# Kernel tuning notes

Hardware: AMD Instinct MI355X
Metric: run time of the kernel (lower is better)

The kernel has to match this reference:

```python
import jax, jax.numpy as jnp
import numpy as np

B, F, T = 4, 2048, 2048
CF, CT = 1024, 1024
H, DH = 16, 64
ALPHA = 1.0 / np.sqrt(DH).astype(np.float32)


def setup_inputs() -> dict:
    key = jax.random.key(0)
    ks = jax.random.split(key, 8)
    s = 0.02  # trunc_normal-ish init scale
    return {
        "from_tensor": jax.random.normal(ks[0], (B, F, CF), jnp.float32),
        "to_tensor": jax.random.normal(ks[1], (B, T, CT), jnp.float32),
        "mask": jax.random.randint(ks[2], (B, F, T), 0, 2, jnp.int32),
        "Wq": jax.random.normal(ks[3], (CF, H * DH), jnp.float32) * s,
        "bq": jnp.zeros((H * DH,), jnp.float32),
        "Wk": jax.random.normal(ks[4], (CT, H * DH), jnp.float32) * s,
        "bk": jnp.zeros((H * DH,), jnp.float32),
        "Wv": jax.random.normal(ks[5], (CT, H * DH), jnp.float32) * s,
        "bv": jnp.zeros((H * DH,), jnp.float32),
    }


def reference(from_tensor, to_tensor, mask, Wq, bq, Wk, bk, Wv, bv):
    # projections (nn.Linear with no activation)
    q = from_tensor @ Wq + bq          # [B,F,H*DH]
    k = to_tensor @ Wk + bk            # [B,T,H*DH]
    v = to_tensor @ Wv + bv            # [B,T,H*DH]
    q = q.reshape(B, F, H, DH)         # query: [..., F, H, DH]
    k = k.reshape(B, T, DH, H)         # key:   [..., T, DH, H]  (self._shape[::-1])
    v = v.reshape(B, T, H, DH)
    # score = transpose(q,-3,-2) @ transpose(k,-3,-1) * alpha -> [B,H,F,T]
    score = jnp.einsum("bfhd,btdh->bhft", q, k) * ALPHA
    if mask is not None:
        adder = (1.0 - mask[:, None].astype(score.dtype)) * -100000.0  # [B,1,F,T]
        score = score + adder
    probs = jax.nn.softmax(score, axis=-1)  # dropout p=0.0 -> identity
    # context = probs @ transpose(v,-3,-2), then transpose back: [B,F,H,DH]
    context = jnp.einsum("bhft,bthd->bfhd", probs, v)
    return context.reshape(B, F, H * DH)
```

## Files before the change

### kernel.cpp

```cpp
#include <hip/hip_runtime.h>
#include <type_traits>

typedef __bf16 bf16_t;
typedef __attribute__((ext_vector_type(8))) __bf16 bf16x8;
typedef __attribute__((ext_vector_type(4))) float f32x4;
typedef __attribute__((ext_vector_type(16))) float f32x16;

__device__ __forceinline__ void async16(const void* g, void* lds) {
  __builtin_amdgcn_global_load_lds((const __attribute__((address_space(1))) unsigned int*)g,
                                   (__attribute__((address_space(3))) unsigned int*)lds, 16, 0, 0);
}

__device__ __forceinline__ unsigned pk2(float lo, float hi) {
  unsigned short a = __builtin_bit_cast(unsigned short, (__bf16)lo);
  unsigned short b = __builtin_bit_cast(unsigned short, (__bf16)hi);
  return (unsigned)a | ((unsigned)b << 16);
}

__device__ __forceinline__ void plswap(unsigned& a, unsigned& b) {
#if __has_builtin(__builtin_amdgcn_permlane32_swap)
  auto r = __builtin_amdgcn_permlane32_swap((int)a, (int)b, false, false);
  a = (unsigned)r[0];
  b = (unsigned)r[1];
#else
  const bool hb = (threadIdx.x & 32) != 0;
  unsigned bx = (unsigned)__shfl_xor((int)b, 32);
  unsigned ax = (unsigned)__shfl_xor((int)a, 32);
  unsigned na = hb ? bx : a;
  unsigned nb = hb ? b : ax;
  a = na; b = nb;
#endif
}

__global__ __launch_bounds__(256) void pack_mask_kernel(const int* __restrict__ mask,
                                                        unsigned long long* __restrict__ mb) {
  const int lane = threadIdx.x & 63, w = threadIdx.x >> 6;
  for (int i = 0; i < 32; ++i) {
    size_t word = (size_t)blockIdx.x * 128 + (size_t)i * 4 + w;
    unsigned long long bits = __ballot(mask[word * 64 + lane] != 0);
    if (lane == 0) mb[word] = bits;
  }
}

__global__ __launch_bounds__(256) void cvt_bf16_kernel(const float* __restrict__ in, bf16_t* __restrict__ out) {
  size_t i = (size_t)blockIdx.x * 256 + threadIdx.x;
  const float4* in4 = (const float4*)in;
  float4 a = in4[i * 2], b = in4[i * 2 + 1];
  bf16x8 o;
  o[0] = (__bf16)a.x; o[1] = (__bf16)a.y; o[2] = (__bf16)a.z; o[3] = (__bf16)a.w;
  o[4] = (__bf16)b.x; o[5] = (__bf16)b.y; o[6] = (__bf16)b.z; o[7] = (__bf16)b.w;
  *(bf16x8*)(out + i * 8) = o;
}

__global__ __launch_bounds__(256) void wt_cvt_kernel(const float* __restrict__ Wq, const float* __restrict__ Wk,
                                                     const float* __restrict__ Wv, bf16_t* __restrict__ Wt) {
  const int z = blockIdx.z;
  const float* src = (z == 0) ? Wq : ((z == 1) ? Wk : Wv);
  const float sc = (z == 0) ? 0.18033688011112042f : 1.0f;
  bf16_t* dst = Wt + (size_t)z * 1024 * 1024;
  const int n = blockIdx.x * 64 + (threadIdx.x & 63);
  const int k8 = blockIdx.y * 4 + (threadIdx.x >> 6);
  bf16x8 o;
#pragma unroll
  for (int j = 0; j < 8; ++j) o[j] = (__bf16)(src[(size_t)(k8 * 8 + j) * 1024 + n] * sc);
  *(bf16x8*)(dst + (size_t)n * 1024 + k8 * 8) = o;
}

__global__ __launch_bounds__(256) void proj_kernel(const bf16_t* __restrict__ A, const bf16_t* __restrict__ Wt,
                                                   const float* __restrict__ bias, bf16_t* __restrict__ dst,
                                                   const int z, const float bscale) {
  __shared__ __align__(16) unsigned char smem[33792];
  bf16_t* se = (bf16_t*)smem;
  const int tid = threadIdx.x, lane = tid & 63, w = tid >> 6;
  const int m0 = blockIdx.x * 128, n0 = blockIdx.y * 128;
  const int wm = (w >> 1) * 64, wn = (w & 1) * 64;
  const int r = lane & 15, kq = lane >> 4;
  const int srow = lane >> 2, sslot = lane & 3;
  f32x4 acc[4][4] = {};

  auto stage = [&](int buf, int k0) {
    bf16_t* Ad = se + buf * 4096;
    bf16_t* Bd = se + 8192 + buf * 4096;
#pragma unroll
    for (int it = 0; it < 2; ++it) {
      const int c = it * 4 + w;
      const int row = c * 16 + srow;
      async16(A + (size_t)(m0 + row) * 1024 + k0 + ((sslot ^ (row & 3)) * 8), Ad + c * 512);
      async16(Wt + (size_t)(n0 + row) * 1024 + k0 + ((sslot ^ (row & 3)) * 8), Bd + c * 512);
    }
  };

  stage(0, 0);
  __syncthreads();
  for (int tile = 0; tile < 32; ++tile) {
    const int cur = tile & 1;
    if (tile < 31) stage(cur ^ 1, (tile + 1) * 32);
    const bf16_t* Al = se + cur * 4096;
    const bf16_t* Bl = se + 8192 + cur * 4096;
    bf16x8 af[4], bfr[4];
#pragma unroll
    for (int i = 0; i < 4; ++i) {
      const int ra = wm + i * 16 + r;
      af[i] = *(const bf16x8*)(Al + ra * 32 + ((kq ^ (ra & 3)) * 8));
      const int rb = wn + i * 16 + r;
      bfr[i] = *(const bf16x8*)(Bl + rb * 32 + ((kq ^ (rb & 3)) * 8));
    }
    __builtin_amdgcn_s_setprio(1);
#pragma unroll
    for (int i = 0; i < 4; ++i)
#pragma unroll
      for (int j = 0; j < 4; ++j)
        acc[i][j] = __builtin_amdgcn_mfma_f32_16x16x32_bf16(af[i], bfr[j], acc[i][j], 0, 0, 0);
    __builtin_amdgcn_s_setprio(0);
    __syncthreads();
  }

  bf16_t* Cl = se;
  float bvv[4];
#pragma unroll
  for (int j = 0; j < 4; ++j) bvv[j] = bias[n0 + wn + j * 16 + r] * bscale;
#pragma unroll
  for (int i = 0; i < 4; ++i)
#pragma unroll
    for (int j = 0; j < 4; ++j)
#pragma unroll
      for (int g = 0; g < 4; ++g)
        Cl[(wm + i * 16 + kq * 4 + g) * 132 + wn + j * 16 + r] = (__bf16)(acc[i][j][g] + bvv[j]);
  __syncthreads();

  const int b = m0 >> 11, sbase = m0 & 2047;
  if (z == 0) {
#pragma unroll
    for (int q = 0; q < 8; ++q) {
      const int cid = q * 256 + tid;
      const int m = cid >> 4, c = (cid >> 3) & 1, d8 = cid & 7;
      bf16x8 val = *(const bf16x8*)(Cl + m * 132 + c * 64 + d8 * 8);
      *(bf16x8*)(dst + ((size_t)(b * 16 + (n0 >> 6) + c) * 2048 + sbase + m) * 64 + d8 * 8) = val;
    }
  } else if (z == 1) {
#pragma unroll
    for (int q = 0; q < 8; ++q) {
      const int cid = q * 256 + tid;
      const int hh = cid >> 7, m = cid & 127;
      bf16x8 val;
#pragma unroll
      for (int dd = 0; dd < 8; ++dd) val[dd] = Cl[m * 132 + dd * 16 + hh];
      *(bf16x8*)(dst + ((size_t)(b * 16 + hh) * 2048 + sbase + m) * 64 + (n0 >> 4)) = val;
    }
  } else {
#pragma unroll
    for (int q = 0; q < 8; ++q) {
      const int cid = q * 256 + tid;
      const int nl = cid >> 4, m8 = cid & 15;
      bf16x8 val;
#pragma unroll
      for (int s = 0; s < 8; ++s) val[s] = Cl[(m8 * 8 + s) * 132 + nl];
      const int hh = (n0 >> 6) + (nl >> 6), dd = nl & 63;
      *(bf16x8*)(dst + ((size_t)(b * 16 + hh) * 64 + dd) * 2048 + sbase + m8 * 8) = val;
    }
  }
}

__global__ __launch_bounds__(256, 2) void attn_kernel(const bf16_t* __restrict__ Q, const bf16_t* __restrict__ K,
                                                      const bf16_t* __restrict__ VT,
                                                      const unsigned long long* __restrict__ mb,
                                                      float* __restrict__ out) {
  __shared__ __align__(16) unsigned char smem[32768];
  bf16_t* se = (bf16_t*)smem;
  const int tid = threadIdx.x, lane = tid & 63, w = tid >> 6;
  const int cl = lane & 31, hi = lane >> 5;
  const int f0 = blockIdx.x * 256, h = blockIdx.y, b = blockIdx.z;
  const size_t bh = (size_t)b * 16 + h;
  const int fw = f0 + w * 64;

  const bf16_t* Qb = Q + (bh * 2048 + fw) * 64;
  bf16x8 qf[2][4];
#pragma unroll
  for (int fb = 0; fb < 2; ++fb)
#pragma unroll
    for (int ks = 0; ks < 4; ++ks)
      qf[fb][ks] = *(const bf16x8*)(Qb + (fb * 32 + cl) * 64 + ks * 16 + hi * 8);

  f32x16 Of[2][2] = {};
  float lacc[2] = {0.f, 0.f};
  bf16x8 paw[2][4];

  const unsigned long long* mrow[2];
  mrow[0] = mb + ((size_t)b * 2048 + fw + cl) * 32;
  mrow[1] = mb + ((size_t)b * 2048 + fw + 32 + cl) * 32;

  const int row8 = lane >> 3, slot = lane & 7;
  const int swz = (slot ^ row8) * 8;
  const bf16_t* kgb[2];
  const bf16_t* vgb[2];
#pragma unroll
  for (int it = 0; it < 2; ++it) {
    const int row = it * 32 + w * 8 + row8;
    kgb[it] = K + (bh * 2048 + row) * 64 + swz;
    vgb[it] = VT + (bh * 64 + row) * 2048 + swz;
  }

  auto stage_k = [&](int buf, int tile) {
    bf16_t* kd = se + buf * 4096 + w * 512;
#pragma unroll
    for (int it = 0; it < 2; ++it)
      async16(kgb[it] + (size_t)tile * 4096, kd + it * 2048);
  };
  auto stage_v = [&](int buf, int tile) {
    bf16_t* vd = se + 8192 + buf * 4096 + w * 512;
#pragma unroll
    for (int it = 0; it < 2; ++it)
      async16(vgb[it] + (size_t)tile * 64, vd + it * 2048);
  };

  auto pv_step = [&](int vbuf) {
    const bf16_t* Vl = se + 8192 + vbuf * 4096;
    __builtin_amdgcn_s_setprio(1);
#pragma unroll
    for (int db = 0; db < 2; ++db) {
      const int vrow0 = db * 32 + cl;
#pragma unroll
      for (int kt = 0; kt < 4; ++kt) {
        bf16x8 vf = *(const bf16x8*)(Vl + vrow0 * 64 + (((2 * kt + hi) ^ (vrow0 & 7)) * 8));
        Of[0][db] = __builtin_amdgcn_mfma_f32_32x32x16_bf16(paw[0][kt], vf, Of[0][db], 0, 0, 0);
        Of[1][db] = __builtin_amdgcn_mfma_f32_32x32x16_bf16(paw[1][kt], vf, Of[1][db], 0, 0, 0);
      }
    }
    __builtin_amdgcn_s_setprio(0);
  };

  unsigned long long mA[2], mB[2];
  stage_k(0, 0);
  mA[0] = mrow[0][0];
  mA[1] = mrow[1][0];
  __syncthreads();

  auto body = [&](auto curc, auto dopvc, unsigned long long (&mc)[2], unsigned long long (&mn)[2], int tile) {
    constexpr int cur = decltype(curc)::value;
    constexpr bool dopv = decltype(dopvc)::value;
    if (tile < 31) {
      stage_k(cur ^ 1, tile + 1);
      mn[0] = mrow[0][tile + 1];
      mn[1] = mrow[1][tile + 1];
    }
    stage_v(cur, tile);
    const bf16_t* Kl = se + cur * 4096;

    f32x16 st0[2], st1[2];
#pragma unroll
    for (int fb = 0; fb < 2; ++fb) {
      const unsigned mw0 = (unsigned)(mc[fb] >> (4 * hi));
      const unsigned mw1 = (unsigned)(mc[fb] >> (32 + 4 * hi));
#pragma unroll
      for (int q = 0; q < 4; ++q)
#pragma unroll
        for (int e = 0; e < 4; ++e) {
          const int idx = q * 4 + e;
          const int pos = e + 8 * q;
          const unsigned s0 = (unsigned)(((int)(mw0 << (31 - pos))) >> 31);
          const unsigned s1 = (unsigned)(((int)(mw1 << (31 - pos))) >> 31);
          st0[fb][idx] = __uint_as_float(~s0 & 0xC6EA6000u);
          st1[fb][idx] = __uint_as_float(~s1 & 0xC6EA6000u);
        }
    }

    {
      const int krow = cl;
      __builtin_amdgcn_s_setprio(1);
#pragma unroll
      for (int ks = 0; ks < 4; ++ks) {
        bf16x8 kf = *(const bf16x8*)(Kl + krow * 64 + (((2 * ks + hi) ^ (krow & 7)) * 8));
        st0[0] = __builtin_amdgcn_mfma_f32_32x32x16_bf16(kf, qf[0][ks], st0[0], 0, 0, 0);
        st0[1] = __builtin_amdgcn_mfma_f32_32x32x16_bf16(kf, qf[1][ks], st0[1], 0, 0, 0);
      }
      __builtin_amdgcn_s_setprio(0);
    }

    if constexpr (dopv) pv_step(cur ^ 1);

    {
      const int krow = 32 + cl;
      __builtin_amdgcn_s_setprio(1);
#pragma unroll
      for (int ks = 0; ks < 4; ++ks) {
        bf16x8 kf = *(const bf16x8*)(Kl + krow * 64 + (((2 * ks + hi) ^ (krow & 7)) * 8));
        st1[0] = __builtin_amdgcn_mfma_f32_32x32x16_bf16(kf, qf[0][ks], st1[0], 0, 0, 0);
        st1[1] = __builtin_amdgcn_mfma_f32_32x32x16_bf16(kf, qf[1][ks], st1[1], 0, 0, 0);
      }
      __builtin_amdgcn_s_setprio(0);
    }

#pragma unroll
    for (int ts = 0; ts < 2; ++ts) {
#pragma unroll
      for (int fb = 0; fb < 2; ++fb) {
        const f32x16& stf = (ts == 0) ? st0[fb] : st1[fb];
        float pv[16];
#pragma unroll
        for (int q = 0; q < 4; ++q)
#pragma unroll
          for (int e = 0; e < 4; ++e) {
            const int idx = q * 4 + e;
            float p = __builtin_amdgcn_exp2f(stf[idx]);
            lacc[fb] += p;
            pv[idx] = p;
          }
#pragma unroll
        for (int kl = 0; kl < 2; ++kl) {
          const int qa = 2 * kl, qb = qa + 1;
          unsigned x0 = pk2(pv[qa * 4 + 0], pv[qa * 4 + 1]);
          unsigned y0 = pk2(pv[qb * 4 + 0], pv[qb * 4 + 1]);
          unsigned x1 = pk2(pv[qa * 4 + 2], pv[qa * 4 + 3]);
          unsigned y1 = pk2(pv[qb * 4 + 2], pv[qb * 4 + 3]);
          plswap(x0, y0);
          plswap(x1, y1);
          union { unsigned u[4]; bf16x8 v; } tmp;
          tmp.u[0] = x0; tmp.u[1] = x1; tmp.u[2] = y0; tmp.u[3] = y1;
          paw[fb][ts * 2 + kl] = tmp.v;
        }
      }
    }
    __syncthreads();
  };

  using c0 = std::integral_constant<int, 0>;
  using c1 = std::integral_constant<int, 1>;
  using bF = std::integral_constant<bool, false>;
  using bT = std::integral_constant<bool, true>;

  body(c0{}, bF{}, mA, mB, 0);
  body(c1{}, bT{}, mB, mA, 1);
  for (int tile = 2; tile < 32; tile += 2) {
    body(c0{}, bT{}, mA, mB, tile);
    body(c1{}, bT{}, mB, mA, tile + 1);
  }
  pv_step(1);

#pragma unroll
  for (int fb = 0; fb < 2; ++fb) lacc[fb] += __shfl_xor(lacc[fb], 32);
  float* lsh = (float*)smem;
  if (hi == 0) {
    lsh[w * 64 + cl] = lacc[0];
    lsh[w * 64 + 32 + cl] = lacc[1];
  }
#pragma unroll
  for (int fb = 0; fb < 2; ++fb)
#pragma unroll
    for (int q = 0; q < 4; ++q)
#pragma unroll
      for (int e = 0; e < 4; ++e) {
        const int idx = q * 4 + e;
        const int row = e + 8 * q + 4 * hi;
        const float li = 1.0f / lsh[w * 64 + fb * 32 + row];
        const size_t orow = ((size_t)b * 2048 + fw + fb * 32 + row) * 1024 + h * 64;
        out[orow + cl] = Of[fb][0][idx] * li;
        out[orow + 32 + cl] = Of[fb][1][idx] * li;
      }
}

extern "C" void kernel_launch(void* const* d_in, const int* in_sizes, int n_in,
                              void* d_out, int out_size, void* d_ws, size_t ws_size,
                              hipStream_t stream) {
  (void)in_sizes; (void)n_in; (void)out_size; (void)ws_size;
  const float* from = (const float*)d_in[0];
  const float* to_  = (const float*)d_in[1];
  const int*   mask = (const int*)d_in[2];
  const float* Wq = (const float*)d_in[3];
  const float* bq = (const float*)d_in[4];
  const float* Wk = (const float*)d_in[5];
  const float* bk = (const float*)d_in[6];
  const float* Wv = (const float*)d_in[7];
  const float* bv = (const float*)d_in[8];
  float* out = (float*)d_out;
  char* ws = (char*)d_ws;

  bf16_t* Qw = (bf16_t*)(ws);
  bf16_t* Kw = (bf16_t*)(ws + (size_t)(1u << 24));
  bf16_t* Vw = (bf16_t*)(ws + (size_t)(2u << 24));
  bf16_t* Wt = (bf16_t*)(ws + (size_t)(3u << 24));
  unsigned long long* mbits = (unsigned long long*)(ws + (size_t)(3u << 24) + (size_t)(6u << 20));
  bf16_t* inb = (bf16_t*)(ws + (size_t)(3u << 24) + (size_t)(8u << 20));

  pack_mask_kernel<<<2048, 256, 0, stream>>>(mask, mbits);
  wt_cvt_kernel<<<dim3(16, 32, 3), 256, 0, stream>>>(Wq, Wk, Wv, Wt);
  cvt_bf16_kernel<<<4096, 256, 0, stream>>>(from, inb);
  proj_kernel<<<dim3(64, 8), 256, 0, stream>>>(inb, Wt, bq, Qw, 0, 0.18033688011112042f);
  cvt_bf16_kernel<<<4096, 256, 0, stream>>>(to_, inb);
  proj_kernel<<<dim3(64, 8), 256, 0, stream>>>(inb, Wt + (1u << 20), bk, Kw, 1, 1.0f);
  proj_kernel<<<dim3(64, 8), 256, 0, stream>>>(inb, Wt + (2u << 20), bv, Vw, 2, 1.0f);
  attn_kernel<<<dim3(8, 16, 4), 256, 0, stream>>>(Qw, Kw, Vw, mbits, out);
}
```

Baseline: 225.1 us.

## Process KV tiles in pairs with four-deep K/V LDS buffering

```diff
diff --git a/kernel.cpp b/kernel.cpp
--- a/kernel.cpp
+++ b/kernel.cpp
@@ -165,7 +165,7 @@
                                                       const bf16_t* __restrict__ VT,
                                                       const unsigned long long* __restrict__ mb,
                                                       float* __restrict__ out) {
-  __shared__ __align__(16) unsigned char smem[32768];
+  __shared__ __align__(16) unsigned char smem[65536];
   bf16_t* se = (bf16_t*)smem;
   const int tid = threadIdx.x, lane = tid & 63, w = tid >> 6;
   const int cl = lane & 31, hi = lane >> 5;
@@ -183,7 +183,7 @@
 
   f32x16 Of[2][2] = {};
   float lacc[2] = {0.f, 0.f};
-  bf16x8 paw[2][4];
+  bf16x8 pawA[2][4], pawB[2][4];
 
   const unsigned long long* mrow[2];
   mrow[0] = mb + ((size_t)b * 2048 + fw + cl) * 32;
@@ -207,50 +207,19 @@
       async16(kgb[it] + (size_t)tile * 4096, kd + it * 2048);
   };
   auto stage_v = [&](int buf, int tile) {
-    bf16_t* vd = se + 8192 + buf * 4096 + w * 512;
+    bf16_t* vd = se + 16384 + buf * 4096 + w * 512;
 #pragma unroll
     for (int it = 0; it < 2; ++it)
       async16(vgb[it] + (size_t)tile * 64, vd + it * 2048);
   };
 
-  auto pv_step = [&](int vbuf) {
-    const bf16_t* Vl = se + 8192 + vbuf * 4096;
-    __builtin_amdgcn_s_setprio(1);
-#pragma unroll
-    for (int db = 0; db < 2; ++db) {
-      const int vrow0 = db * 32 + cl;
-#pragma unroll
-      for (int kt = 0; kt < 4; ++kt) {
-        bf16x8 vf = *(const bf16x8*)(Vl + vrow0 * 64 + (((2 * kt + hi) ^ (vrow0 & 7)) * 8));
-        Of[0][db] = __builtin_amdgcn_mfma_f32_32x32x16_bf16(paw[0][kt], vf, Of[0][db], 0, 0, 0);
-        Of[1][db] = __builtin_amdgcn_mfma_f32_32x32x16_bf16(paw[1][kt], vf, Of[1][db], 0, 0, 0);
-      }
-    }
-    __builtin_amdgcn_s_setprio(0);
-  };
-
-  unsigned long long mA[2], mB[2];
-  stage_k(0, 0);
-  mA[0] = mrow[0][0];
-  mA[1] = mrow[1][0];
-  __syncthreads();
-
-  auto body = [&](auto curc, auto dopvc, unsigned long long (&mc)[2], unsigned long long (&mn)[2], int tile) {
-    constexpr int cur = decltype(curc)::value;
-    constexpr bool dopv = decltype(dopvc)::value;
-    if (tile < 31) {
-      stage_k(cur ^ 1, tile + 1);
-      mn[0] = mrow[0][tile + 1];
-      mn[1] = mrow[1][tile + 1];
-    }
-    stage_v(cur, tile);
-    const bf16_t* Kl = se + cur * 4096;
-
-    f32x16 st0[2], st1[2];
+  auto cinit = [&](const unsigned long long mwt0, const unsigned long long mwt1,
+                   f32x16 (&st0)[2], f32x16 (&st1)[2]) {
+    const unsigned long long mwt[2] = {mwt0, mwt1};
 #pragma unroll
     for (int fb = 0; fb < 2; ++fb) {
-      const unsigned mw0 = (unsigned)(mc[fb] >> (4 * hi));
-      const unsigned mw1 = (unsigned)(mc[fb] >> (32 + 4 * hi));
+      const unsigned mw0 = (unsigned)(mwt[fb] >> (4 * hi));
+      const unsigned mw1 = (unsigned)(mwt[fb] >> (32 + 4 * hi));
 #pragma unroll
       for (int q = 0; q < 4; ++q)
 #pragma unroll
@@ -263,33 +232,32 @@
           st1[fb][idx] = __uint_as_float(~s1 & 0xC6EA6000u);
         }
     }
-
+  };
+
+  auto qk = [&](const bf16_t* Kl, f32x16 (&st0)[2], f32x16 (&st1)[2]) {
+    __builtin_amdgcn_s_setprio(1);
     {
       const int krow = cl;
-      __builtin_amdgcn_s_setprio(1);
 #pragma unroll
       for (int ks = 0; ks < 4; ++ks) {
         bf16x8 kf = *(const bf16x8*)(Kl + krow * 64 + (((2 * ks + hi) ^ (krow & 7)) * 8));
         st0[0] = __builtin_amdgcn_mfma_f32_32x32x16_bf16(kf, qf[0][ks], st0[0], 0, 0, 0);
         st0[1] = __builtin_amdgcn_mfma_f32_32x32x16_bf16(kf, qf[1][ks], st0[1], 0, 0, 0);
       }
-      __builtin_amdgcn_s_setprio(0);
-    }
-
-    if constexpr (dopv) pv_step(cur ^ 1);
-
+    }
     {
       const int krow = 32 + cl;
-      __builtin_amdgcn_s_setprio(1);
 #pragma unroll
       for (int ks = 0; ks < 4; ++ks) {
         bf16x8 kf = *(const bf16x8*)(Kl + krow * 64 + (((2 * ks + hi) ^ (krow & 7)) * 8));
         st1[0] = __builtin_amdgcn_mfma_f32_32x32x16_bf16(kf, qf[0][ks], st1[0], 0, 0, 0);
         st1[1] = __builtin_amdgcn_mfma_f32_32x32x16_bf16(kf, qf[1][ks], st1[1], 0, 0, 0);
       }
-      __builtin_amdgcn_s_setprio(0);
-    }
-
+    }
+    __builtin_amdgcn_s_setprio(0);
+  };
+
+  auto sm = [&](const f32x16 (&st0)[2], const f32x16 (&st1)[2], bf16x8 (&paw)[2][4]) {
 #pragma unroll
     for (int ts = 0; ts < 2; ++ts) {
 #pragma unroll
@@ -320,21 +288,57 @@
         }
       }
     }
+  };
+
+  auto pv_step = [&](int vbuf, const bf16x8 (&paw)[2][4]) {
+    const bf16_t* Vl = se + 16384 + vbuf * 4096;
+    __builtin_amdgcn_s_setprio(1);
+#pragma unroll
+    for (int db = 0; db < 2; ++db) {
+      const int vrow0 = db * 32 + cl;
+#pragma unroll
+      for (int kt = 0; kt < 4; ++kt) {
+        bf16x8 vf = *(const bf16x8*)(Vl + vrow0 * 64 + (((2 * kt + hi) ^ (vrow0 & 7)) * 8));
+        Of[0][db] = __builtin_amdgcn_mfma_f32_32x32x16_bf16(paw[0][kt], vf, Of[0][db], 0, 0, 0);
+        Of[1][db] = __builtin_amdgcn_mfma_f32_32x32x16_bf16(paw[1][kt], vf, Of[1][db], 0, 0, 0);
+      }
+    }
+    __builtin_amdgcn_s_setprio(0);
+  };
+
+  unsigned long long mA[2][2], mB[2][2];
+  stage_k(0, 0); stage_v(0, 0);
+  stage_k(1, 1); stage_v(1, 1);
+  mA[0][0] = mrow[0][0]; mA[1][0] = mrow[1][0];
+  mA[0][1] = mrow[0][1]; mA[1][1] = mrow[1][1];
+  __syncthreads();
+
+  auto pair = [&](auto ppc, unsigned long long (&mc)[2][2], unsigned long long (&mn)[2][2], int tile) {
+    constexpr int cb = decltype(ppc)::value * 2;
+    if (tile < 30) {
+      stage_k(cb ^ 2, tile + 2); stage_v(cb ^ 2, tile + 2);
+      stage_k((cb ^ 2) + 1, tile + 3); stage_v((cb ^ 2) + 1, tile + 3);
+      mn[0][0] = mrow[0][tile + 2]; mn[1][0] = mrow[1][tile + 2];
+      mn[0][1] = mrow[0][tile + 3]; mn[1][1] = mrow[1][tile + 3];
+    }
+    f32x16 stA0[2], stA1[2], stB0[2], stB1[2];
+    cinit(mc[0][0], mc[1][0], stA0, stA1);
+    qk(se + cb * 4096, stA0, stA1);
+    cinit(mc[0][1], mc[1][1], stB0, stB1);
+    qk(se + (cb + 1) * 4096, stB0, stB1);
+    sm(stA0, stA1, pawA);
+    pv_step(cb, pawA);
+    sm(stB0, stB1, pawB);
+    pv_step(cb + 1, pawB);
     __syncthreads();
   };
 
   using c0 = std::integral_constant<int, 0>;
   using c1 = std::integral_constant<int, 1>;
-  using bF = std::integral_constant<bool, false>;
-  using bT = std::integral_constant<bool, true>;
-
-  body(c0{}, bF{}, mA, mB, 0);
-  body(c1{}, bT{}, mB, mA, 1);
-  for (int tile = 2; tile < 32; tile += 2) {
-    body(c0{}, bT{}, mA, mB, tile);
-    body(c1{}, bT{}, mB, mA, tile + 1);
-  }
-  pv_step(1);
+  for (int t = 0; t < 32; t += 4) {
+    pair(c0{}, mA, mB, t);
+    pair(c1{}, mB, mA, t + 2);
+  }
 
 #pragma unroll
   for (int fb = 0; fb < 2; ++fb) lacc[fb] += __shfl_xor(lacc[fb], 32);
```

Result: slower. 272.8 us (+21.2%).
